# Kernel tuning notes

Hardware: AMD Instinct MI355X
Metric: run time of the kernel (lower is better)

## Reference

```python
import jax, jax.numpy as jnp
import numpy as np

LR = 0.1  # forward default lr; noise_std=0.0 default so no Langevin noise
B, DX, DY, H, K = 65536, 256, 64, 512, 4


def setup_inputs() -> dict:
    key = jax.random.key(0)
    ks = jax.random.split(key, 8)
    x = jax.random.normal(ks[0], (B, DX), dtype=jnp.float32)
    t = jax.random.randint(ks[1], (B,), 0, K, dtype=jnp.int64)
    # MLP params, Kaiming-ish scaling
    s1 = 1.0 / np.sqrt(DX + DY)
    s2 = 1.0 / np.sqrt(H)
    W1 = jax.random.normal(ks[2], (DX + DY, H), dtype=jnp.float32) * s1
    b1 = jnp.zeros((H,), jnp.float32)
    W2 = jax.random.normal(ks[3], (H, H), dtype=jnp.float32) * s2
    b2 = jnp.zeros((H,), jnp.float32)
    W3 = jax.random.normal(ks[4], (H, K), dtype=jnp.float32) * s2
    b3 = jnp.zeros((K,), jnp.float32)
    return {"x": x, "t": t, "W1": W1, "b1": b1, "W2": W2, "b2": b2,
            "W3": W3, "b3": b3, "steps": 20}


def reference(x, t, W1, b1, W2, b2, W3, b3, steps):
    # gather index: t.clamp_min(0) -> [B, 1]
    tc = jnp.clip(t, 0, None).astype(jnp.int32)[:, None]
    d_y = W1.shape[0] - x.shape[1]

    def energy_sum(y):
        h = jax.nn.relu(jnp.concatenate([x, y], axis=-1) @ W1 + b1)
        h = jax.nn.relu(h @ W2 + b2)
        e = h @ W3 + b3                      # [B, K]
        return jnp.take_along_axis(e, tc, axis=1).sum()

    grad_e = jax.grad(energy_sum)

    def step(y, _):
        return y - LR * grad_e(y), None

    y0 = jnp.zeros((x.shape[0], d_y), dtype=x.dtype)
    y_final, _ = jax.lax.scan(step, y0, None, length=steps)
    return y_final
```

## Files before the change

### kernel.cpp

```cpp
#include <hip/hip_runtime.h>

typedef _Float16 f16x8 __attribute__((ext_vector_type(8)));
typedef float f32x4 __attribute__((ext_vector_type(4)));

#define HID   512
#define DXD   256
#define DYD   64
#define NROWS 64
#define NTHR  1024
#define LRC   0.1f
#define TAU1  1e-4f
#define TAU2  1e-4f
#define SC12  2.44140625e-4f

#define OFF_W1YB 0
#define OFF_W1Y4 32768
#define OFF_W2B  65536
#define OFF_W2B3 327680
#define PH       589824

#define L_H0  0
#define L_H1  65536
#define HPL   65536
#define L_Y0  131072
#define L_Y1  139264
#define YPL   8192
#define L_TL  147456
#define SMEM_BYTES 147712

__device__ __forceinline__ void f2h2(float v, unsigned short* ph, unsigned short* pm) {
    unsigned short hb, mb;
    if (fabsf(v) >= 6.103515625e-05f) {
        _Float16 h = (_Float16)v;
        _Float16 m = (_Float16)((v - (float)h) * 4096.0f);
        hb = __builtin_bit_cast(unsigned short, h);
        mb = __builtin_bit_cast(unsigned short, m);
    } else {
        _Float16 m = (_Float16)(v * 4096.0f);
        hb = 0;
        mb = __builtin_bit_cast(unsigned short, m);
    }
    *ph = hb; *pm = mb;
}

template<int KSTEPS, int SROWA, int KDIM, int APL_>
__device__ __forceinline__ void gemmh1(const char* ldsA, const unsigned short* B,
                                       int l4, int l16, int ct,
                                       f32x4 acc[4], f32x4 accm[4])
{
    const int cb0 = l4 * 16;
    #pragma unroll
    for (int kk = 0; kk < KSTEPS; ++kk) {
        const int cb = kk * 64 + cb0;
        f16x8 ah[4], am[4];
        #pragma unroll
        for (int mt = 0; mt < 4; ++mt) {
            const int row = mt * 16 + l16;
            const int off = row * SROWA + (cb ^ ((row & 7) << 4));
            ah[mt] = *(const f16x8*)(ldsA + off);
            am[mt] = *(const f16x8*)(ldsA + APL_ + off);
        }
        const size_t off = (size_t)(ct * 16 + l16) * (KDIM * 2) + cb;
        f16x8 bh = *(const f16x8*)((const char*)B + off);
        f16x8 bm = *(const f16x8*)((const char*)(B + PH) + off);
        #pragma unroll
        for (int mt = 0; mt < 4; ++mt) {
            acc[mt]  = __builtin_amdgcn_mfma_f32_16x16x32_f16(ah[mt], bh, acc[mt],  0, 0, 0);
            accm[mt] = __builtin_amdgcn_mfma_f32_16x16x32_f16(ah[mt], bm, accm[mt], 0, 0, 0);
            accm[mt] = __builtin_amdgcn_mfma_f32_16x16x32_f16(am[mt], bh, accm[mt], 0, 0, 0);
        }
    }
}

__device__ __attribute__((noinline))
float rescue_s2(const char* smem, int row, int col, float b2n,
                const unsigned short* __restrict__ wsb) {
    float r = b2n;
    const int xr = (row & 7) << 4;
    const int rb = row * 1024;
    const char* wh = (const char*)(wsb + OFF_W2B) + (size_t)col * 1024;
    const char* wm = (const char*)(wsb + PH + OFF_W2B) + (size_t)col * 1024;
    for (int j0 = 0; j0 < HID; j0 += 8) {
        const int off = rb + ((j0 * 2) ^ xr);
        f16x8 h  = *(const f16x8*)(smem + L_H0 + off);
        f16x8 m_ = *(const f16x8*)(smem + L_H1 + off);
        f16x8 bh = *(const f16x8*)(wh + j0 * 2);
        f16x8 bm = *(const f16x8*)(wm + j0 * 2);
        #pragma unroll
        for (int u = 0; u < 8; ++u) {
            float hv = (float)h[u]  + (float)m_[u] * SC12;
            float wv = (float)bh[u] + (float)bm[u] * SC12;
            r = fmaf(hv, wv, r);
        }
    }
    return r;
}

__device__ __attribute__((noinline))
float rescue_s1(const char* smem, int row, int col, float cval,
                const unsigned short* __restrict__ wsb) {
    float r = cval;
    const int xr = (row & 7) << 4;
    const int rb = row * 128;
    const char* wh = (const char*)(wsb + OFF_W1YB) + (size_t)col * 128;
    const char* wm = (const char*)(wsb + PH + OFF_W1YB) + (size_t)col * 128;
    for (int j0 = 0; j0 < DYD; j0 += 8) {
        const int off = rb + ((j0 * 2) ^ xr);
        f16x8 h  = *(const f16x8*)(smem + L_Y0 + off);
        f16x8 m_ = *(const f16x8*)(smem + L_Y1 + off);
        f16x8 bh = *(const f16x8*)(wh + j0 * 2);
        f16x8 bm = *(const f16x8*)(wm + j0 * 2);
        #pragma unroll
        for (int u = 0; u < 8; ++u) {
            float yv = (float)h[u]  + (float)m_[u] * SC12;
            float wv = (float)bh[u] + (float)bm[u] * SC12;
            r = fmaf(yv, wv, r);
        }
    }
    return r;
}

__global__ void wconv(const float* __restrict__ W1, const float* __restrict__ W2,
                      unsigned short* __restrict__ wsb)
{
    int i = blockIdx.x * blockDim.x + threadIdx.x;
    if (i >= PH) return;
    float v;
    if (i < OFF_W1Y4)      { int n = i >> 6, k = i & 63;                    v = W1[(256 + k) * 512 + n]; }
    else if (i < OFF_W2B)  { int j = i - OFF_W1Y4, d = j >> 9, k = j & 511; v = W1[(256 + d) * 512 + k]; }
    else if (i < OFF_W2B3) { int j = i - OFF_W2B,  n = j >> 9, k = j & 511; v = W2[k * 512 + n]; }
    else                   { int j = i - OFF_W2B3, n = j >> 9, k = j & 511; v = W2[n * 512 + k]; }
    f2h2(v, &wsb[i], &wsb[i + PH]);
}

__global__ __attribute__((amdgpu_flat_work_group_size(NTHR, NTHR), amdgpu_waves_per_eu(4, 4)))
void ebm_mfma(const float* __restrict__ x, const int* __restrict__ tt,
              const float* __restrict__ W1, const float* __restrict__ b1,
              const float* __restrict__ W2, const float* __restrict__ b2,
              const float* __restrict__ W3, const int* __restrict__ stepsp,
              const unsigned short* __restrict__ wsb, float* __restrict__ out)
{
    __shared__ __align__(16) char smem[SMEM_BYTES];

    const int tid  = threadIdx.x;
    const int w    = tid >> 6, lane = tid & 63;
    const int l4   = lane >> 4, l16 = lane & 15;
    const int r0   = blockIdx.x * NROWS;
    const int nt0  = w * 2;
    const int nsteps = *stepsp;

    if (tid < NROWS) {
        int tv = tt[r0 + tid];
        ((int*)(smem + L_TL))[tid] = tv < 0 ? 0 : tv;
    }
    for (int i = tid; i < 2 * YPL / 4; i += NTHR) ((unsigned*)(smem + L_Y0))[i] = 0u;

    {
        const float4* xg = (const float4*)(x + (size_t)r0 * DXD);
        #pragma unroll
        for (int j = 0; j < 4; ++j) {
            int i4 = j * NTHR + tid;
            ((float4*)(smem + L_H0))[i4] = xg[i4];
        }
    }
    __syncthreads();

    f32x4 c_reg[4][2];
    {
        float bb[2];
        #pragma unroll
        for (int nq = 0; nq < 2; ++nq) bb[nq] = b1[(nt0 + nq) * 16 + l16];
        #pragma unroll
        for (int mt = 0; mt < 4; ++mt)
            #pragma unroll
            for (int nq = 0; nq < 2; ++nq)
                c_reg[mt][nq] = (f32x4){bb[nq], bb[nq], bb[nq], bb[nq]};
        for (int i = 0; i < DXD; i += 4) {
            float wv[4][2];
            #pragma unroll
            for (int d = 0; d < 4; ++d)
                #pragma unroll
                for (int nq = 0; nq < 2; ++nq)
                    wv[d][nq] = W1[(size_t)(i + d) * HID + (nt0 + nq) * 16 + l16];
            #pragma unroll
            for (int mt = 0; mt < 4; ++mt)
                #pragma unroll
                for (int q = 0; q < 4; ++q) {
                    const int row = mt * 16 + l4 * 4 + q;
                    float4 xv = *(const float4*)(smem + L_H0 + row * 1024 + i * 4);
                    #pragma unroll
                    for (int nq = 0; nq < 2; ++nq) {
                        c_reg[mt][nq][q] = fmaf(xv.x, wv[0][nq], c_reg[mt][nq][q]);
                        c_reg[mt][nq][q] = fmaf(xv.y, wv[1][nq], c_reg[mt][nq][q]);
                        c_reg[mt][nq][q] = fmaf(xv.z, wv[2][nq], c_reg[mt][nq][q]);
                        c_reg[mt][nq][q] = fmaf(xv.w, wv[3][nq], c_reg[mt][nq][q]);
                    }
                }
        }
    }

    float b2v[2];
    #pragma unroll
    for (int nq = 0; nq < 2; ++nq) b2v[nq] = b2[(nt0 + nq) * 16 + l16];

    const int mt4 = w >> 2;
    const int nt4 = w & 3;
    f32x4 ym = (f32x4){0.f, 0.f, 0.f, 0.f};

    for (int s = 0; s < nsteps; ++s) {
        __syncthreads();

        unsigned mk = 0u;
        #pragma unroll
        for (int nq = 0; nq < 2; ++nq) {
            f32x4 acc[4], accm[4];
            #pragma unroll
            for (int mt = 0; mt < 4; ++mt) { acc[mt] = c_reg[mt][nq]; accm[mt] = (f32x4){0.f,0.f,0.f,0.f}; }
            gemmh1<2, 128, 64, YPL>(smem + L_Y0, wsb + OFF_W1YB, l4, l16, nt0 + nq, acc, accm);
            const int col = (nt0 + nq) * 16 + l16;
            f32x4 v4[4];
            unsigned tie = 0u;
            #pragma unroll
            for (int mt = 0; mt < 4; ++mt) {
                #pragma unroll
                for (int q = 0; q < 4; ++q) {
                    const int row = mt * 16 + l4 * 4 + q;
                    float v = acc[mt][q] + accm[mt][q] * SC12;
                    v4[mt][q] = v;
                    if (fabsf(v) < TAU1) tie |= 1u << (mt * 4 + q);
                    const int off = row * 1024 + ((col * 2) ^ ((row & 7) << 4));
                    if (v > 0.f) {
                        mk |= 1u << ((mt * 2 + nq) * 4 + q);
                        f2h2(v, (unsigned short*)(smem + L_H0 + off), (unsigned short*)(smem + L_H1 + off));
                    } else {
                        *(unsigned short*)(smem + L_H0 + off) = 0;
                        *(unsigned short*)(smem + L_H1 + off) = 0;
                    }
                }
            }
            if (__builtin_expect(tie != 0u, 0)) {
                #pragma unroll
                for (int mt = 0; mt < 4; ++mt) {
                    #pragma unroll
                    for (int q = 0; q < 4; ++q) {
                        if ((tie >> (mt * 4 + q)) & 1u) {
                            const int row = mt * 16 + l4 * 4 + q;
                            const float vr = rescue_s1(smem, row, col, c_reg[mt][nq][q], wsb);
                            const int off = row * 1024 + ((col * 2) ^ ((row & 7) << 4));
                            const unsigned bit = 1u << ((mt * 2 + nq) * 4 + q);
                            if (vr > 0.f) {
                                mk |= bit;
                                f2h2(vr, (unsigned short*)(smem + L_H0 + off), (unsigned short*)(smem + L_H1 + off));
                            } else {
                                mk &= ~bit;
                                *(unsigned short*)(smem + L_H0 + off) = 0;
                                *(unsigned short*)(smem + L_H1 + off) = 0;
                            }
                        }
                    }
                }
            }
            __builtin_amdgcn_sched_barrier(0);
        }
        __syncthreads();

        unsigned pos2 = 0u;
        #pragma unroll
        for (int nq = 0; nq < 2; ++nq) {
            f32x4 acc[4], accm[4];
            #pragma unroll
            for (int mt = 0; mt < 4; ++mt) { acc[mt] = (f32x4){b2v[nq],b2v[nq],b2v[nq],b2v[nq]}; accm[mt] = (f32x4){0.f,0.f,0.f,0.f}; }
            gemmh1<16, 1024, 512, HPL>(smem + L_H0, wsb + OFF_W2B, l4, l16, nt0 + nq, acc, accm);
            const int col = (nt0 + nq) * 16 + l16;
            unsigned tie = 0u;
            #pragma unroll
            for (int mt = 0; mt < 4; ++mt) {
                #pragma unroll
                for (int q = 0; q < 4; ++q) {
                    float v = acc[mt][q] + accm[mt][q] * SC12;
                    if (fabsf(v) < TAU2) tie |= 1u << (mt * 4 + q);
                    if (v > 0.f) pos2 |= 1u << ((mt * 2 + nq) * 4 + q);
                }
            }
            if (__builtin_expect(tie != 0u, 0)) {
                #pragma unroll
                for (int mt = 0; mt < 4; ++mt) {
                    #pragma unroll
                    for (int q = 0; q < 4; ++q) {
                        if ((tie >> (mt * 4 + q)) & 1u) {
                            const int row = mt * 16 + l4 * 4 + q;
                            const float vr = rescue_s2(smem, row, col, b2v[nq], wsb);
                            const unsigned bit = 1u << ((mt * 2 + nq) * 4 + q);
                            if (vr > 0.f) pos2 |= bit; else pos2 &= ~bit;
                        }
                    }
                }
            }
            __builtin_amdgcn_sched_barrier(0);
        }
        __syncthreads();

        #pragma unroll
        for (int mt = 0; mt < 4; ++mt) {
            #pragma unroll
            for (int nq = 0; nq < 2; ++nq) {
                const int col = (nt0 + nq) * 16 + l16;
                #pragma unroll
                for (int q = 0; q < 4; ++q) {
                    const int row = mt * 16 + l4 * 4 + q;
                    const int tv = ((const int*)(smem + L_TL))[row];
                    const int off = row * 1024 + ((col * 2) ^ ((row & 7) << 4));
                    if ((pos2 >> ((mt * 2 + nq) * 4 + q)) & 1u) {
                        f2h2(W3[col * 4 + tv],
                             (unsigned short*)(smem + L_H0 + off),
                             (unsigned short*)(smem + L_H1 + off));
                    } else {
                        *(unsigned short*)(smem + L_H0 + off) = 0;
                        *(unsigned short*)(smem + L_H1 + off) = 0;
                    }
                }
            }
        }
        __syncthreads();

        f32x4 g2vA[4], g2vB[4];
        {
            f32x4 acc[4], accm[4];
            #pragma unroll
            for (int mt = 0; mt < 4; ++mt) { acc[mt] = (f32x4){0.f,0.f,0.f,0.f}; accm[mt] = (f32x4){0.f,0.f,0.f,0.f}; }
            gemmh1<16, 1024, 512, HPL>(smem + L_H0, wsb + OFF_W2B3, l4, l16, nt0 + 0, acc, accm);
            #pragma unroll
            for (int mt = 0; mt < 4; ++mt)
                #pragma unroll
                for (int q = 0; q < 4; ++q)
                    g2vA[mt][q] = acc[mt][q] + accm[mt][q] * SC12;
        }
        __builtin_amdgcn_sched_barrier(0);
        {
            f32x4 acc[4], accm[4];
            #pragma unroll
            for (int mt = 0; mt < 4; ++mt) { acc[mt] = (f32x4){0.f,0.f,0.f,0.f}; accm[mt] = (f32x4){0.f,0.f,0.f,0.f}; }
            gemmh1<16, 1024, 512, HPL>(smem + L_H0, wsb + OFF_W2B3, l4, l16, nt0 + 1, acc, accm);
            #pragma unroll
            for (int mt = 0; mt < 4; ++mt)
                #pragma unroll
                for (int q = 0; q < 4; ++q)
                    g2vB[mt][q] = acc[mt][q] + accm[mt][q] * SC12;
        }
        __syncthreads();

        #pragma unroll
        for (int mt = 0; mt < 4; ++mt) {
            {
                const int col2 = ((nt0 + 0) * 16 + l16) * 2;
                #pragma unroll
                for (int q = 0; q < 4; ++q) {
                    const int row = mt * 16 + l4 * 4 + q;
                    const int off = row * 1024 + (col2 ^ ((row & 7) << 4));
                    if ((mk >> ((mt * 2 + 0) * 4 + q)) & 1u) {
                        f2h2(g2vA[mt][q],
                             (unsigned short*)(smem + L_H0 + off),
                             (unsigned short*)(smem + L_H1 + off));
                    } else {
                        *(unsigned short*)(smem + L_H0 + off) = 0;
                        *(unsigned short*)(smem + L_H1 + off) = 0;
                    }
                }
            }
            {
                const int col2 = ((nt0 + 1) * 16 + l16) * 2;
                #pragma unroll
                for (int q = 0; q < 4; ++q) {
                    const int row = mt * 16 + l4 * 4 + q;
                    const int off = row * 1024 + (col2 ^ ((row & 7) << 4));
                    if ((mk >> ((mt * 2 + 1) * 4 + q)) & 1u) {
                        f2h2(g2vB[mt][q],
                             (unsigned short*)(smem + L_H0 + off),
                             (unsigned short*)(smem + L_H1 + off));
                    } else {
                        *(unsigned short*)(smem + L_H0 + off) = 0;
                        *(unsigned short*)(smem + L_H1 + off) = 0;
                    }
                }
            }
        }
        __syncthreads();

        f32x4 gA = (f32x4){0.f, 0.f, 0.f, 0.f}, gAm = gA;
        {
            const char* bh = (const char*)(wsb + OFF_W1Y4);
            const char* bm = (const char*)(wsb + PH + OFF_W1Y4);
            #pragma unroll
            for (int kk = 0; kk < 16; ++kk) {
                const int cb = kk * 64 + l4 * 16;
                const int row = mt4 * 16 + l16;
                const int offA = row * 1024 + (cb ^ ((row & 7) << 4));
                f16x8 ah = *(const f16x8*)(smem + L_H0 + offA);
                f16x8 am = *(const f16x8*)(smem + L_H1 + offA);
                const size_t obA = (size_t)(nt4 * 16 + l16) * 1024 + cb;
                f16x8 bAh = *(const f16x8*)(bh + obA);
                f16x8 bAm = *(const f16x8*)(bm + obA);
                gA  = __builtin_amdgcn_mfma_f32_16x16x32_f16(ah, bAh, gA,  0, 0, 0);
                gAm = __builtin_amdgcn_mfma_f32_16x16x32_f16(ah, bAm, gAm, 0, 0, 0);
                gAm = __builtin_amdgcn_mfma_f32_16x16x32_f16(am, bAh, gAm, 0, 0, 0);
            }
        }
        #pragma unroll
        for (int q = 0; q < 4; ++q)
            ym[q] = ym[q] - LRC * (gA[q] + gAm[q] * SC12);
        #pragma unroll
        for (int q = 0; q < 4; ++q) {
            const int row = mt4 * 16 + l4 * 4 + q;
            const int col = nt4 * 16 + l16;
            const int off = row * 128 + ((col * 2) ^ ((row & 7) << 4));
            f2h2(ym[q], (unsigned short*)(smem + L_Y0 + off),
                        (unsigned short*)(smem + L_Y1 + off));
        }
    }

    #pragma unroll
    for (int q = 0; q < 4; ++q) {
        const int row = mt4 * 16 + l4 * 4 + q;
        const int col = nt4 * 16 + l16;
        out[(size_t)(r0 + row) * DYD + col] = ym[q];
    }
}

extern "C" void kernel_launch(void* const* d_in, const int* in_sizes, int n_in,
                              void* d_out, int out_size, void* d_ws, size_t ws_size,
                              hipStream_t stream) {
    const float* x  = (const float*)d_in[0];
    const int*   t  = (const int*)d_in[1];
    const float* W1 = (const float*)d_in[2];
    const float* b1 = (const float*)d_in[3];
    const float* W2 = (const float*)d_in[4];
    const float* b2 = (const float*)d_in[5];
    const float* W3 = (const float*)d_in[6];
    const int* steps = (const int*)d_in[8];
    float* out = (float*)d_out;
    unsigned short* wsb = (unsigned short*)d_ws;

    const int B = in_sizes[0] / DXD;
    const int nblocks = B / NROWS;

    wconv<<<(PH + 255) / 256, 256, 0, stream>>>(W1, W2, wsb);

    ebm_mfma<<<nblocks, NTHR, 0, stream>>>(x, t, W1, b1, W2, b2, W3, steps, wsb, out);
}
```

Before: 26.53 ms.

## Halve rows per block to 32 and give each wave four column tiles

Shrinks each workgroup from 64 rows/1024 threads to 32 rows/512 threads, halving LDS use so more blocks can be resident per CU. Each wave now covers 4 column tiles over 2 row tiles instead of 2 over 4, which changes the MFMA tiling and the register layout of the carried x·W1 partials. The tradeoff is that each B-fragment load from global/L2 weights is reused across only 2 row tiles instead of 4, so weight traffic per row doubles.

```diff
diff --git a/kernel.cpp b/kernel.cpp
--- a/kernel.cpp
+++ b/kernel.cpp
@@ -6,8 +6,8 @@
 #define HID   512
 #define DXD   256
 #define DYD   64
-#define NROWS 64
-#define NTHR  1024
+#define NROWS 32
+#define NTHR  512
 #define LRC   0.1f
 #define TAU1  1e-4f
 #define TAU2  1e-4f
@@ -20,13 +20,13 @@
 #define PH       589824
 
 #define L_H0  0
-#define L_H1  65536
-#define HPL   65536
-#define L_Y0  131072
-#define L_Y1  139264
-#define YPL   8192
-#define L_TL  147456
-#define SMEM_BYTES 147712
+#define L_H1  32768
+#define HPL   32768
+#define L_Y0  65536
+#define L_Y1  69632
+#define YPL   4096
+#define L_TL  73728
+#define SMEM_BYTES 73856
 
 __device__ __forceinline__ void f2h2(float v, unsigned short* ph, unsigned short* pm) {
     unsigned short hb, mb;
@@ -43,18 +43,18 @@
     *ph = hb; *pm = mb;
 }
 
-template<int KSTEPS, int SROWA, int KDIM, int APL_>
+template<int MT, int KSTEPS, int SROWA, int KDIM, int APL_>
 __device__ __forceinline__ void gemmh1(const char* ldsA, const unsigned short* B,
                                        int l4, int l16, int ct,
-                                       f32x4 acc[4], f32x4 accm[4])
+                                       f32x4 acc[MT], f32x4 accm[MT])
 {
     const int cb0 = l4 * 16;
     #pragma unroll
     for (int kk = 0; kk < KSTEPS; ++kk) {
         const int cb = kk * 64 + cb0;
-        f16x8 ah[4], am[4];
-        #pragma unroll
-        for (int mt = 0; mt < 4; ++mt) {
+        f16x8 ah[MT], am[MT];
+        #pragma unroll
+        for (int mt = 0; mt < MT; ++mt) {
             const int row = mt * 16 + l16;
             const int off = row * SROWA + (cb ^ ((row & 7) << 4));
             ah[mt] = *(const f16x8*)(ldsA + off);
@@ -64,7 +64,7 @@
         f16x8 bh = *(const f16x8*)((const char*)B + off);
         f16x8 bm = *(const f16x8*)((const char*)(B + PH) + off);
         #pragma unroll
-        for (int mt = 0; mt < 4; ++mt) {
+        for (int mt = 0; mt < MT; ++mt) {
             acc[mt]  = __builtin_amdgcn_mfma_f32_16x16x32_f16(ah[mt], bh, acc[mt],  0, 0, 0);
             accm[mt] = __builtin_amdgcn_mfma_f32_16x16x32_f16(ah[mt], bm, accm[mt], 0, 0, 0);
             accm[mt] = __builtin_amdgcn_mfma_f32_16x16x32_f16(am[mt], bh, accm[mt], 0, 0, 0);
@@ -133,7 +133,7 @@
     f2h2(v, &wsb[i], &wsb[i + PH]);
 }
 
-__global__ __attribute__((amdgpu_flat_work_group_size(NTHR, NTHR), amdgpu_waves_per_eu(4, 4)))
+__global__ __launch_bounds__(NTHR, 4)
 void ebm_mfma(const float* __restrict__ x, const int* __restrict__ tt,
               const float* __restrict__ W1, const float* __restrict__ b1,
               const float* __restrict__ W2, const float* __restrict__ b2,
@@ -146,7 +146,7 @@
     const int w    = tid >> 6, lane = tid & 63;
     const int l4   = lane >> 4, l16 = lane & 15;
     const int r0   = blockIdx.x * NROWS;
-    const int nt0  = w * 2;
+    const int nt0  = w * 4;
     const int nsteps = *stepsp;
 
     if (tid < NROWS) {
@@ -165,31 +165,31 @@
     }
     __syncthreads();
 
-    f32x4 c_reg[4][2];
+    f32x4 c_reg[2][4];
     {
-        float bb[2];
-        #pragma unroll
-        for (int nq = 0; nq < 2; ++nq) bb[nq] = b1[(nt0 + nq) * 16 + l16];
-        #pragma unroll
-        for (int mt = 0; mt < 4; ++mt)
-            #pragma unroll
-            for (int nq = 0; nq < 2; ++nq)
+        float bb[4];
+        #pragma unroll
+        for (int nq = 0; nq < 4; ++nq) bb[nq] = b1[(nt0 + nq) * 16 + l16];
+        #pragma unroll
+        for (int mt = 0; mt < 2; ++mt)
+            #pragma unroll
+            for (int nq = 0; nq < 4; ++nq)
                 c_reg[mt][nq] = (f32x4){bb[nq], bb[nq], bb[nq], bb[nq]};
         for (int i = 0; i < DXD; i += 4) {
-            float wv[4][2];
+            float wv[4][4];
             #pragma unroll
             for (int d = 0; d < 4; ++d)
                 #pragma unroll
-                for (int nq = 0; nq < 2; ++nq)
+                for (int nq = 0; nq < 4; ++nq)
                     wv[d][nq] = W1[(size_t)(i + d) * HID + (nt0 + nq) * 16 + l16];
             #pragma unroll
-            for (int mt = 0; mt < 4; ++mt)
+            for (int mt = 0; mt < 2; ++mt)
                 #pragma unroll
                 for (int q = 0; q < 4; ++q) {
                     const int row = mt * 16 + l4 * 4 + q;
                     float4 xv = *(const float4*)(smem + L_H0 + row * 1024 + i * 4);
                     #pragma unroll
-                    for (int nq = 0; nq < 2; ++nq) {
+                    for (int nq = 0; nq < 4; ++nq) {
                         c_reg[mt][nq][q] = fmaf(xv.x, wv[0][nq], c_reg[mt][nq][q]);
                         c_reg[mt][nq][q] = fmaf(xv.y, wv[1][nq], c_reg[mt][nq][q]);
                         c_reg[mt][nq][q] = fmaf(xv.z, wv[2][nq], c_reg[mt][nq][q]);
@@ -199,9 +199,9 @@
         }
     }
 
-    float b2v[2];
+    float b2v[4];
     #pragma unroll
-    for (int nq = 0; nq < 2; ++nq) b2v[nq] = b2[(nt0 + nq) * 16 + l16];
+    for (int nq = 0; nq < 4; ++nq) b2v[nq] = b2[(nt0 + nq) * 16 + l16];
 
     const int mt4 = w >> 2;
     const int nt4 = w & 3;
@@ -212,25 +212,23 @@
 
         unsigned mk = 0u;
         #pragma unroll
-        for (int nq = 0; nq < 2; ++nq) {
-            f32x4 acc[4], accm[4];
-            #pragma unroll
-            for (int mt = 0; mt < 4; ++mt) { acc[mt] = c_reg[mt][nq]; accm[mt] = (f32x4){0.f,0.f,0.f,0.f}; }
-            gemmh1<2, 128, 64, YPL>(smem + L_Y0, wsb + OFF_W1YB, l4, l16, nt0 + nq, acc, accm);
+        for (int nq = 0; nq < 4; ++nq) {
+            f32x4 acc[2], accm[2];
+            #pragma unroll
+            for (int mt = 0; mt < 2; ++mt) { acc[mt] = c_reg[mt][nq]; accm[mt] = (f32x4){0.f,0.f,0.f,0.f}; }
+            gemmh1<2, 2, 128, 64, YPL>(smem + L_Y0, wsb + OFF_W1YB, l4, l16, nt0 + nq, acc, accm);
             const int col = (nt0 + nq) * 16 + l16;
-            f32x4 v4[4];
             unsigned tie = 0u;
             #pragma unroll
-            for (int mt = 0; mt < 4; ++mt) {
+            for (int mt = 0; mt < 2; ++mt) {
                 #pragma unroll
                 for (int q = 0; q < 4; ++q) {
                     const int row = mt * 16 + l4 * 4 + q;
                     float v = acc[mt][q] + accm[mt][q] * SC12;
-                    v4[mt][q] = v;
                     if (fabsf(v) < TAU1) tie |= 1u << (mt * 4 + q);
                     const int off = row * 1024 + ((col * 2) ^ ((row & 7) << 4));
                     if (v > 0.f) {
-                        mk |= 1u << ((mt * 2 + nq) * 4 + q);
+                        mk |= 1u << ((mt * 4 + nq) * 4 + q);
                         f2h2(v, (unsigned short*)(smem + L_H0 + off), (unsigned short*)(smem + L_H1 + off));
                     } else {
                         *(unsigned short*)(smem + L_H0 + off) = 0;
@@ -240,14 +238,14 @@
             }
             if (__builtin_expect(tie != 0u, 0)) {
                 #pragma unroll
-                for (int mt = 0; mt < 4; ++mt) {
+                for (int mt = 0; mt < 2; ++mt) {
                     #pragma unroll
                     for (int q = 0; q < 4; ++q) {
                         if ((tie >> (mt * 4 + q)) & 1u) {
                             const int row = mt * 16 + l4 * 4 + q;
                             const float vr = rescue_s1(smem, row, col, c_reg[mt][nq][q], wsb);
                             const int off = row * 1024 + ((col * 2) ^ ((row & 7) << 4));
-                            const unsigned bit = 1u << ((mt * 2 + nq) * 4 + q);
+                            const unsigned bit = 1u << ((mt * 4 + nq) * 4 + q);
                             if (vr > 0.f) {
                                 mk |= bit;
                                 f2h2(vr, (unsigned short*)(smem + L_H0 + off), (unsigned short*)(smem + L_H1 + off));
@@ -266,31 +264,31 @@
 
         unsigned pos2 = 0u;
         #pragma unroll
-        for (int nq = 0; nq < 2; ++nq) {
-            f32x4 acc[4], accm[4];
-            #pragma unroll
-            for (int mt = 0; mt < 4; ++mt) { acc[mt] = (f32x4){b2v[nq],b2v[nq],b2v[nq],b2v[nq]}; accm[mt] = (f32x4){0.f,0.f,0.f,0.f}; }
-            gemmh1<16, 1024, 512, HPL>(smem + L_H0, wsb + OFF_W2B, l4, l16, nt0 + nq, acc, accm);
+        for (int nq = 0; nq < 4; ++nq) {
+            f32x4 acc[2], accm[2];
+            #pragma unroll
+            for (int mt = 0; mt < 2; ++mt) { acc[mt] = (f32x4){b2v[nq],b2v[nq],b2v[nq],b2v[nq]}; accm[mt] = (f32x4){0.f,0.f,0.f,0.f}; }
+            gemmh1<2, 16, 1024, 512, HPL>(smem + L_H0, wsb + OFF_W2B, l4, l16, nt0 + nq, acc, accm);
             const int col = (nt0 + nq) * 16 + l16;
             unsigned tie = 0u;
             #pragma unroll
-            for (int mt = 0; mt < 4; ++mt) {
+            for (int mt = 0; mt < 2; ++mt) {
                 #pragma unroll
                 for (int q = 0; q < 4; ++q) {
                     float v = acc[mt][q] + accm[mt][q] * SC12;
                     if (fabsf(v) < TAU2) tie |= 1u << (mt * 4 + q);
-                    if (v > 0.f) pos2 |= 1u << ((mt * 2 + nq) * 4 + q);
+                    if (v > 0.f) pos2 |= 1u << ((mt * 4 + nq) * 4 + q);
                 }
             }
             if (__builtin_expect(tie != 0u, 0)) {
                 #pragma unroll
-                for (int mt = 0; mt < 4; ++mt) {
+                for (int mt = 0; mt < 2; ++mt) {
                     #pragma unroll
                     for (int q = 0; q < 4; ++q) {
                         if ((tie >> (mt * 4 + q)) & 1u) {
                             const int row = mt * 16 + l4 * 4 + q;
                             const float vr = rescue_s2(smem, row, col, b2v[nq], wsb);
-                            const unsigned bit = 1u << ((mt * 2 + nq) * 4 + q);
+                            const unsigned bit = 1u << ((mt * 4 + nq) * 4 + q);
                             if (vr > 0.f) pos2 |= bit; else pos2 &= ~bit;
                         }
                     }
@@ -301,16 +299,16 @@
         __syncthreads();
 
         #pragma unroll
-        for (int mt = 0; mt < 4; ++mt) {
-            #pragma unroll
-            for (int nq = 0; nq < 2; ++nq) {
+        for (int mt = 0; mt < 2; ++mt) {
+            #pragma unroll
+            for (int nq = 0; nq < 4; ++nq) {
                 const int col = (nt0 + nq) * 16 + l16;
                 #pragma unroll
                 for (int q = 0; q < 4; ++q) {
                     const int row = mt * 16 + l4 * 4 + q;
                     const int tv = ((const int*)(smem + L_TL))[row];
                     const int off = row * 1024 + ((col * 2) ^ ((row & 7) << 4));
-                    if ((pos2 >> ((mt * 2 + nq) * 4 + q)) & 1u) {
+                    if ((pos2 >> ((mt * 4 + nq) * 4 + q)) & 1u) {
                         f2h2(W3[col * 4 + tv],
                              (unsigned short*)(smem + L_H0 + off),
                              (unsigned short*)(smem + L_H1 + off));
@@ -323,58 +321,33 @@
         }
         __syncthreads();
 
-        f32x4 g2vA[4], g2vB[4];
-        {
-            f32x4 acc[4], accm[4];
-            #pragma unroll
-            for (int mt = 0; mt < 4; ++mt) { acc[mt] = (f32x4){0.f,0.f,0.f,0.f}; accm[mt] = (f32x4){0.f,0.f,0.f,0.f}; }
-            gemmh1<16, 1024, 512, HPL>(smem + L_H0, wsb + OFF_W2B3, l4, l16, nt0 + 0, acc, accm);
-            #pragma unroll
-            for (int mt = 0; mt < 4; ++mt)
+        f32x4 g2v[2][4];
+        #pragma unroll
+        for (int nq = 0; nq < 4; ++nq) {
+            f32x4 acc[2], accm[2];
+            #pragma unroll
+            for (int mt = 0; mt < 2; ++mt) { acc[mt] = (f32x4){0.f,0.f,0.f,0.f}; accm[mt] = (f32x4){0.f,0.f,0.f,0.f}; }
+            gemmh1<2, 16, 1024, 512, HPL>(smem + L_H0, wsb + OFF_W2B3, l4, l16, nt0 + nq, acc, accm);
+            #pragma unroll
+            for (int mt = 0; mt < 2; ++mt)
                 #pragma unroll
                 for (int q = 0; q < 4; ++q)
-                    g2vA[mt][q] = acc[mt][q] + accm[mt][q] * SC12;
-        }
-        __builtin_amdgcn_sched_barrier(0);
-        {
-            f32x4 acc[4], accm[4];
-            #pragma unroll
-            for (int mt = 0; mt < 4; ++mt) { acc[mt] = (f32x4){0.f,0.f,0.f,0.f}; accm[mt] = (f32x4){0.f,0.f,0.f,0.f}; }
-            gemmh1<16, 1024, 512, HPL>(smem + L_H0, wsb + OFF_W2B3, l4, l16, nt0 + 1, acc, accm);
-            #pragma unroll
-            for (int mt = 0; mt < 4; ++mt)
-                #pragma unroll
-                for (int q = 0; q < 4; ++q)
-                    g2vB[mt][q] = acc[mt][q] + accm[mt][q] * SC12;
-        }
-        __syncthreads();
-
-        #pragma unroll
-        for (int mt = 0; mt < 4; ++mt) {
-            {
-                const int col2 = ((nt0 + 0) * 16 + l16) * 2;
+                    g2v[mt][nq][q] = acc[mt][q] + accm[mt][q] * SC12;
+            __builtin_amdgcn_sched_barrier(0);
+        }
+        __syncthreads();
+
+        #pragma unroll
+        for (int mt = 0; mt < 2; ++mt) {
+            #pragma unroll
+            for (int nq = 0; nq < 4; ++nq) {
+                const int col2 = ((nt0 + nq) * 16 + l16) * 2;
                 #pragma unroll
                 for (int q = 0; q < 4; ++q) {
                     const int row = mt * 16 + l4 * 4 + q;
                     const int off = row * 1024 + (col2 ^ ((row & 7) << 4));
-                    if ((mk >> ((mt * 2 + 0) * 4 + q)) & 1u) {
-                        f2h2(g2vA[mt][q],
-                             (unsigned short*)(smem + L_H0 + off),
-                             (unsigned short*)(smem + L_H1 + off));
-                    } else {
-                        *(unsigned short*)(smem + L_H0 + off) = 0;
-                        *(unsigned short*)(smem + L_H1 + off) = 0;
-                    }
-                }
-            }
-            {
-                const int col2 = ((nt0 + 1) * 16 + l16) * 2;
-                #pragma unroll
-                for (int q = 0; q < 4; ++q) {
-                    const int row = mt * 16 + l4 * 4 + q;
-                    const int off = row * 1024 + (col2 ^ ((row & 7) << 4));
-                    if ((mk >> ((mt * 2 + 1) * 4 + q)) & 1u) {
-                        f2h2(g2vB[mt][q],
+                    if ((mk >> ((mt * 4 + nq) * 4 + q)) & 1u) {
+                        f2h2(g2v[mt][nq][q],
                              (unsigned short*)(smem + L_H0 + off),
                              (unsigned short*)(smem + L_H1 + off));
                     } else {
```

New measurement: 30.92 ms. 1.17x slower.
